# Optimization experiments

Hardware: AMD Instinct MI355X
Metric: run time of the kernel (lower is better)

Reference implementation:

```python
import jax, jax.numpy as jnp
import numpy as np

SIGMA = 25.0
N, E, F, D = 10000, 160000, 256, 3


def setup_inputs() -> dict:
    key = jax.random.key(0)
    ks = jax.random.split(key, 24)
    s = 0.02
    inp = {
        "x": jax.random.normal(ks[0], (N, D), jnp.float32),
        "edge_index": jax.random.randint(ks[1], (2, E), 0, N, jnp.int64),
        "t": jax.random.uniform(ks[2], (N, 1), jnp.float32, 1e-3, 1.0),
        "emb_pcs": jax.random.normal(ks[3], (N, F), jnp.float32),
        # x_encoder
        "enc_W": jax.random.normal(ks[4], (D, F), jnp.float32) * s,
        "enc_b": jnp.zeros((F,), jnp.float32),
        # GaussianFourierProjection (scale=30, fixed) + Linear
        "fourier_W": jax.random.normal(ks[5], (F // 2,), jnp.float32) * 30.0,
        "te_W": jax.random.normal(ks[6], (F, F), jnp.float32) * s,
        "te_b": jnp.zeros((F,), jnp.float32),
        # mlp1 / mlp2: Linear(6F,F) -> ReLU -> Linear(F,F)
        "m1_W1": jax.random.normal(ks[7], (6 * F, F), jnp.float32) * s,
        "m1_b1": jnp.zeros((F,), jnp.float32),
        "m1_W2": jax.random.normal(ks[8], (F, F), jnp.float32) * s,
        "m1_b2": jnp.zeros((F,), jnp.float32),
        "m2_W1": jax.random.normal(ks[9], (6 * F, F), jnp.float32) * s,
        "m2_b1": jnp.zeros((F,), jnp.float32),
        "m2_W2": jax.random.normal(ks[10], (F, F), jnp.float32) * s,
        "m2_b2": jnp.zeros((F,), jnp.float32),
        # mlp3: Linear(6F,F) -> ReLU -> Linear(F,D)
        "m3_W1": jax.random.normal(ks[11], (6 * F, F), jnp.float32) * s,
        "m3_b1": jnp.zeros((F,), jnp.float32),
        "m3_W2": jax.random.normal(ks[12], (F, D), jnp.float32) * s,
        "m3_b2": jnp.zeros((D,), jnp.float32),
    }
    return inp


def _edge_conv(h, src, dst, W1, b1, W2, b2, n):
    # PyG EdgeConv: out_i = max_{j->i} MLP([x_i, x_j - x_i])
    hi = h[dst]                                             # [E, 3F]
    e = jnp.concatenate([hi, h[src] - hi], axis=-1)         # [E, 6F]
    e = jax.nn.relu(e @ W1 + b1) @ W2 + b2                  # [E, out]
    out = jax.ops.segment_max(e, dst, num_segments=n)
    return jnp.where(jnp.isfinite(out), out, 0.0)           # empty segments -> 0


def reference(x, edge_index, t, emb_pcs,
              enc_W, enc_b, fourier_W, te_W, te_b,
              m1_W1, m1_b1, m1_W2, m1_b2,
              m2_W1, m2_b1, m2_W2, m2_b2,
              m3_W1, m3_b1, m3_W2, m3_b2):
    src, dst = edge_index[0], edge_index[1]
    n = x.shape[0]
    # time embedding: Fourier projection -> Linear -> swish
    tv = t[:, 0]
    proj = tv[:, None] * fourier_W[None, :] * (2.0 * np.pi)  # [N, F/2]
    temb = jnp.concatenate([jnp.sin(proj), jnp.cos(proj)], axis=-1) @ te_W + te_b
    temb = temb * jax.nn.sigmoid(temb)                       # [N, F]
    h = x @ enc_W + enc_b                                    # [N, F]
    h = jnp.concatenate([h, temb, emb_pcs], axis=-1)         # [N, 3F]
    h = jax.nn.relu(_edge_conv(h, src, dst, m1_W1, m1_b1, m1_W2, m1_b2, n))
    h = jnp.concatenate([h, temb, emb_pcs], axis=-1)
    h = jax.nn.relu(_edge_conv(h, src, dst, m2_W1, m2_b1, m2_W2, m2_b2, n))
    h = jnp.concatenate([h, temb, emb_pcs], axis=-1)
    h = _edge_conv(h, src, dst, m3_W1, m3_b1, m3_W2, m3_b2, n)  # [N, D]
    # marginal_prob_std(t) = sqrt((sigma^(2t) - 1) / (2 ln sigma))
    std = jnp.sqrt((jnp.power(SIGMA, 2.0 * t) - 1.0) / (2.0 * jnp.log(SIGMA)))
    return h / (std + 1e-7)
```

## Files before the change

kernel.cpp:

```cpp
#include <hip/hip_runtime.h>
#include <hip/hip_bf16.h>
#include <math.h>

#define HC 768
#define DPB 8

typedef __attribute__((ext_vector_type(8))) short bf16x8;
typedef __attribute__((ext_vector_type(4))) float f32x4;

__device__ __forceinline__ float bf2f(unsigned short h) {
    return __uint_as_float(((unsigned)h) << 16);
}
__device__ __forceinline__ unsigned short f2bf(float f) {
    unsigned u = __float_as_uint(f);
    return (unsigned short)((u + 0x7fffu + ((u >> 16) & 1u)) >> 16);
}
__device__ __forceinline__ unsigned pack_bf2(float a, float b) {
    __hip_bfloat162 h = __float22bfloat162_rn(make_float2(a, b));
    return *reinterpret_cast<unsigned*>(&h);
}

__device__ __forceinline__ unsigned enc_f(float f) {
    unsigned u = __float_as_uint(f);
    return (u & 0x80000000u) ? ~u : (u | 0x80000000u);
}
__device__ __forceinline__ float dec_f(unsigned e) {
    unsigned u = (e & 0x80000000u) ? (e & 0x7FFFFFFFu) : ~e;
    return __uint_as_float(u);
}
#define ENC_NEG_INF 0x007FFFFFu

__global__ void pre_and_prep_kernel(const float* __restrict__ x,
                                    const float* __restrict__ t,
                                    const float* __restrict__ emb,
                                    const float* __restrict__ enc_W,
                                    const float* __restrict__ enc_b,
                                    const float* __restrict__ fw,
                                    const float* __restrict__ te_W,
                                    const float* __restrict__ te_b,
                                    unsigned short* __restrict__ hcat,
                                    float* __restrict__ invstd,
                                    const float* __restrict__ W1a,
                                    const float* __restrict__ W1b,
                                    const float* __restrict__ W1c,
                                    const float* __restrict__ W2a,
                                    const float* __restrict__ W2b,
                                    const float* __restrict__ W2c,
                                    unsigned short* __restrict__ WcatT,
                                    unsigned short* __restrict__ W2T,
                                    unsigned short* __restrict__ W2T3,
                                    int N, int nPre) {
    __shared__ float smem[64 * 65];
    const int tid = threadIdx.x;

    if ((int)blockIdx.x < nPre) {
        float (*ti)[256] = (float(*)[256])smem;
        float* tv = smem + 8 * 256;
        const int n0 = blockIdx.x * 8;

        if (tid < 8) {
            int n = n0 + tid;
            float tt = (n < N) ? t[n] : 1.0f;
            tv[tid] = tt;
            const float ln_s = 3.2188758248682006f;
            float p = expf(2.0f * tt * ln_s);
            float sd = sqrtf((p - 1.0f) / (2.0f * ln_s));
            if (n < N) invstd[n] = 1.0f / (sd + 1e-7f);
        }
        __syncthreads();

        const float TWO_PI = 6.283185307179586f;
        for (int p = tid; p < 8 * 128; p += 256) {
            int n = p >> 7, j = p & 127;
            float pr = tv[n] * fw[j] * TWO_PI;
            ti[n][j]       = sinf(pr);
            ti[n][j + 128] = cosf(pr);
        }
        __syncthreads();

        const int j = tid;
        float acc[8];
#pragma unroll
        for (int n = 0; n < 8; ++n) acc[n] = 0.f;
        for (int k = 0; k < 256; ++k) {
            float w = te_W[k * 256 + j];
#pragma unroll
            for (int n = 0; n < 8; ++n) acc[n] += ti[n][k] * w;
        }
        float bj  = te_b[j];
        float ew0 = enc_W[0 * 256 + j], ew1 = enc_W[1 * 256 + j], ew2 = enc_W[2 * 256 + j];
        float ebj = enc_b[j];
        for (int n = 0; n < 8; ++n) {
            int node = n0 + n;
            if (node >= N) break;
            float v = acc[n] + bj;
            float temb = v / (1.0f + expf(-v));
            float h0 = x[node * 3 + 0] * ew0 + x[node * 3 + 1] * ew1 +
                       x[node * 3 + 2] * ew2 + ebj;
            hcat[(size_t)node * HC + j]       = f2bf(h0);
            hcat[(size_t)node * HC + 256 + j] = f2bf(temb);
            hcat[(size_t)node * HC + 512 + j] = f2bf(emb[node * 256 + j]);
        }
    } else {
        float (*buf)[65] = (float(*)[65])smem;
        const int bid = blockIdx.x - nPre;
        const int tx = tid & 63, ty = tid >> 6;

        if (bid < 288) {
            const int l = bid / 96, r = bid - l * 96;
            const float* W1 = (l == 0) ? W1a : (l == 1) ? W1b : W1c;
            unsigned short* WT = WcatT + (size_t)l * 512 * 768;
            const int k0 = (r % 12) * 64, n0 = (r / 12) * 64;
#pragma unroll
            for (int i = 0; i < 16; ++i) {
                int kl = ty + i * 4;
                int k = k0 + kl, n = n0 + tx;
                float v = (n < 256) ? (W1[(size_t)k * 256 + n] - W1[(size_t)(k + 768) * 256 + n])
                                    : W1[(size_t)(k + 768) * 256 + (n - 256)];
                buf[kl][tx] = v;
            }
            __syncthreads();
#pragma unroll
            for (int i = 0; i < 16; ++i) {
                int nl = ty + i * 4;
                WT[(size_t)(n0 + nl) * 768 + k0 + tx] = f2bf(buf[tx][nl]);
            }
        } else if (bid < 320) {
            const int m = bid - 288, l = m >> 4, r = m & 15;
            const float* W2 = (l == 0) ? W2a : W2b;
            unsigned short* WT = W2T + (size_t)l * 256 * 256;
            const int k0 = (r & 3) * 64, n0 = (r >> 2) * 64;
#pragma unroll
            for (int i = 0; i < 16; ++i) {
                int kl = ty + i * 4;
                buf[kl][tx] = W2[(size_t)(k0 + kl) * 256 + n0 + tx];
            }
            __syncthreads();
#pragma unroll
            for (int i = 0; i < 16; ++i) {
                int nl = ty + i * 4;
                WT[(size_t)(n0 + nl) * 256 + k0 + tx] = f2bf(buf[tx][nl]);
            }
        } else {
            int idx = (bid - 320) * 256 + tid;
            int n = idx >> 8, k = idx & 255;
            W2T3[idx] = (n < 3) ? f2bf(W2c[(size_t)k * 3 + n]) : (unsigned short)0;
        }
    }
}

__global__ __launch_bounds__(256)
void node_gemm_mfma_kernel(const unsigned short* __restrict__ A,
                           const unsigned short* __restrict__ BT,
                           const float* __restrict__ b1,
                           unsigned short* __restrict__ C,
                           int M) {
    const int row0 = blockIdx.x * 64, col0 = blockIdx.y * 128;
    const int tid = threadIdx.x;
    const int wv = tid >> 6, lane = tid & 63;
    const int q = lane >> 4, nl = lane & 15;

    int row = row0 + wv * 16 + nl;
    int rowc = (row < M) ? row : (M - 1);
    const unsigned short* pa = A + (size_t)rowc * HC + q * 8;

    f32x4 acc[8];
#pragma unroll
    for (int t = 0; t < 8; ++t) acc[t] = (f32x4){0.f, 0.f, 0.f, 0.f};

    for (int ks = 0; ks < 24; ++ks) {
        const int k0 = ks * 32;
        const bf16x8 av = *(const bf16x8*)(pa + k0);
#pragma unroll
        for (int t = 0; t < 8; ++t) {
            const bf16x8 bv = *(const bf16x8*)(BT + (size_t)(col0 + t * 16 + nl) * 768 + k0 + q * 8);
            acc[t] = __builtin_amdgcn_mfma_f32_16x16x32_bf16(av, bv, acc[t], 0, 0, 0);
        }
    }

    const int r0 = row0 + wv * 16 + q * 4;
#pragma unroll
    for (int t = 0; t < 8; ++t) {
        int col = col0 + t * 16 + nl;
        float bb = (col < 256) ? b1[col] : 0.f;
#pragma unroll
        for (int i = 0; i < 4; ++i) {
            int r = r0 + i;
            if (r < M) C[(size_t)r * 512 + col] = f2bf(acc[t][i] + bb);
        }
    }
}

__global__ void init_kernel(unsigned* __restrict__ cnt, unsigned* __restrict__ seg3, int N) {
    int idx = blockIdx.x * 256 + threadIdx.x;
    if (idx < 2 * N) cnt[idx] = 0u;
    else if (idx < 5 * N) seg3[idx - 2 * N] = ENC_NEG_INF;
}
__global__ void hist_kernel(const int* __restrict__ dst, unsigned* __restrict__ cnt, int E) {
    int e = blockIdx.x * 256 + threadIdx.x;
    if (e < E) atomicAdd(&cnt[dst[e]], 1u);
}
__global__ void scan_kernel(const unsigned* __restrict__ cnt,
                            int* __restrict__ row_start, int N) {
    __shared__ unsigned buf[1024];
    __shared__ unsigned carry;
    const int tid = threadIdx.x;
    if (tid == 0) carry = 0u;
    __syncthreads();
    for (int base = 0; base < N; base += 1024) {
        int i = base + tid;
        unsigned v = (i < N) ? cnt[i] : 0u;
        buf[tid] = v;
        __syncthreads();
#pragma unroll
        for (int off = 1; off < 1024; off <<= 1) {
            unsigned add = (tid >= off) ? buf[tid - off] : 0u;
            __syncthreads();
            buf[tid] += add;
            __syncthreads();
        }
        if (i < N) row_start[i] = (int)(carry + buf[tid] - v);
        __syncthreads();
        if (tid == 0) carry += buf[1023];
        __syncthreads();
    }
    if (tid == 0) row_start[N] = (int)carry;
}
__global__ void scatter_kernel(const int* __restrict__ src, const int* __restrict__ dst,
                               const int* __restrict__ row_start,
                               unsigned* __restrict__ wcnt,
                               int* __restrict__ es, int* __restrict__ ed, int E) {
    int e = blockIdx.x * 256 + threadIdx.x;
    if (e >= E) return;
    int d = dst[e];
    int pos = row_start[d] + (int)atomicAdd(&wcnt[d], 1u);
    es[pos] = src[e];
    ed[pos] = d;
}

__global__ __launch_bounds__(256, 3)
void edge_seg_gemm_kernel(const unsigned short* __restrict__ RQb,
                          const int* __restrict__ es,
                          const int* __restrict__ ed,
                          const int* __restrict__ row_start,
                          const unsigned short* __restrict__ W2T,
                          const float* __restrict__ b2,
                          unsigned short* __restrict__ hcat,
                          int N, int E) {
    __shared__ unsigned short af2[32 * 64 * 8];
    __shared__ unsigned short rdst[DPB][264];
    __shared__ unsigned lseg[DPB * 256];
    __shared__ int ss[64], sdl[64];
    const int d0 = blockIdx.x * DPB;
    const int tid = threadIdx.x;
    const int wv = tid >> 6, lane = tid & 63;
    const int q = lane >> 4, nl = lane & 15;

    for (int i = tid; i < DPB * 256; i += 256) lseg[i] = ENC_NEG_INF;

    {
        int rrow = tid >> 5;
        int kc = (tid & 31) * 8;
        int d = d0 + rrow;
        int dc = (d < N) ? d : (N - 1);
        *(bf16x8*)&rdst[rrow][kc] = *(const bf16x8*)(RQb + (size_t)dc * 512 + kc);
    }

    const int eBeg = row_start[d0];
    const int eEnd = row_start[min(d0 + DPB, N)];

    for (int c0 = eBeg; c0 < eEnd; c0 += 64) {
        __syncthreads();
        if (tid < 64) {
            int e = c0 + tid;
            ss[tid]  = (e < eEnd) ? es[e] : 0;
            sdl[tid] = (e < eEnd) ? (ed[e] - d0) : -1;
        }
        __syncthreads();

        {
            const int el = tid >> 2;
            const int kc = (tid & 3) * 64;
            int dl = sdl[el];
            int dla = (dl >= 0) ? dl : 0;
            int srow = ss[el];
            const unsigned short* ps = RQb + (size_t)srow * 512 + 256;
#pragma unroll
            for (int j = 0; j < 8; ++j) {
                const int k = kc + j * 8;
                bf16x8 dv = *(const bf16x8*)&rdst[dla][k];
                bf16x8 sv = *(const bf16x8*)(ps + k);
                float f[8];
#pragma unroll
                for (int u = 0; u < 8; ++u)
                    f[u] = fmaxf(bf2f((unsigned short)dv[u]) + bf2f((unsigned short)sv[u]), 0.f);
                uint4 o;
                o.x = pack_bf2(f[0], f[1]);
                o.y = pack_bf2(f[2], f[3]);
                o.z = pack_bf2(f[4], f[5]);
                o.w = pack_bf2(f[6], f[7]);
                *(uint4*)&af2[((k >> 3) * 64 + el) * 8] = o;
            }
        }
        __syncthreads();

#pragma unroll
        for (int sub = 0; sub < 4; ++sub) {
            f32x4 acc[4];
#pragma unroll
            for (int t = 0; t < 4; ++t) acc[t] = (f32x4){0.f, 0.f, 0.f, 0.f};
#pragma unroll
            for (int ks = 0; ks < 8; ++ks) {
                const bf16x8 av = *(const bf16x8*)&af2[((ks * 4 + q) * 64 + sub * 16 + nl) * 8];
#pragma unroll
                for (int t = 0; t < 4; ++t) {
                    const bf16x8 bv = *(const bf16x8*)(W2T +
                        (size_t)(wv * 64 + t * 16 + nl) * 256 + ks * 32 + q * 8);
                    acc[t] = __builtin_amdgcn_mfma_f32_16x16x32_bf16(av, bv, acc[t], 0, 0, 0);
                }
            }
            const int m0 = sub * 16 + q * 4;
            int dls[4];
#pragma unroll
            for (int i = 0; i < 4; ++i) dls[i] = sdl[m0 + i];
#pragma unroll
            for (int t = 0; t < 4; ++t) {
                const int col = wv * 64 + t * 16 + nl;
                float cur = -INFINITY;
                int cd = dls[0];
#pragma unroll
                for (int i = 0; i < 4; ++i) {
                    int dl = dls[i];
                    if (dl != cd) {
                        if (cd >= 0) atomicMax(&lseg[cd * 256 + col], enc_f(cur));
                        cur = -INFINITY; cd = dl;
                    }
                    cur = fmaxf(cur, acc[t][i]);
                }
                if (cd >= 0) atomicMax(&lseg[cd * 256 + col], enc_f(cur));
            }
        }
    }
    __syncthreads();

    for (int i = tid; i < DPB * 256; i += 256) {
        int dl = i >> 8, col = i & 255;
        int d = d0 + dl;
        if (d >= N) continue;
        float f = dec_f(lseg[i]);
        float v = isfinite(f) ? fmaxf(f + b2[col], 0.f) : 0.f;
        hcat[(size_t)d * HC + col] = f2bf(v);
    }
}

__global__ __launch_bounds__(256)
void edge3_mfma_kernel(const unsigned short* __restrict__ RQb,
                       const int* __restrict__ es,
                       const int* __restrict__ ed,
                       const unsigned short* __restrict__ W2T3,
                       const float* __restrict__ b2,
                       unsigned* __restrict__ seg3,
                       int E) {
    const int wave = blockIdx.x * 4 + (threadIdx.x >> 6);
    const int lane = threadIdx.x & 63;
    const int q = lane >> 4, nl = lane & 15;
    const int e0 = wave * 16;
    if (e0 >= E) return;

    bf16x8 bv[8];
#pragma unroll
    for (int ks = 0; ks < 8; ++ks)
        bv[ks] = *(const bf16x8*)(W2T3 + (size_t)nl * 256 + ks * 32 + q * 8);

    int eA = e0 + nl;
    int eAc = (eA < E) ? eA : (E - 1);
    const int dA = ed[eAc], sA = es[eAc];
    const unsigned short* pd = RQb + (size_t)dA * 512 + q * 8;
    const unsigned short* ps = RQb + (size_t)sA * 512 + 256 + q * 8;

    f32x4 acc = (f32x4){0.f, 0.f, 0.f, 0.f};
#pragma unroll
    for (int ks = 0; ks < 8; ++ks) {
        bf16x8 dv = *(const bf16x8*)(pd + ks * 32);
        bf16x8 sv = *(const bf16x8*)(ps + ks * 32);
        float f[8];
#pragma unroll
        for (int u = 0; u < 8; ++u)
            f[u] = fmaxf(bf2f((unsigned short)dv[u]) + bf2f((unsigned short)sv[u]), 0.f);
        uint4 o;
        o.x = pack_bf2(f[0], f[1]);
        o.y = pack_bf2(f[2], f[3]);
        o.z = pack_bf2(f[4], f[5]);
        o.w = pack_bf2(f[6], f[7]);
        bf16x8 av = *(bf16x8*)&o;
        acc = __builtin_amdgcn_mfma_f32_16x16x32_bf16(av, bv[ks], acc, 0, 0, 0);
    }

    if (nl < 3) {
        float bb = b2[nl];
        float cur = -INFINITY;
        int cd = -2;
#pragma unroll
        for (int i = 0; i < 4; ++i) {
            int e = e0 + q * 4 + i;
            int d = (e < E) ? ed[e] : -1;
            if (d != cd) {
                if (cd >= 0) atomicMax(&seg3[(size_t)cd * 3 + nl], enc_f(cur + bb));
                cur = -INFINITY; cd = d;
            }
            if (d >= 0) cur = fmaxf(cur, acc[i]);
        }
        if (cd >= 0) atomicMax(&seg3[(size_t)cd * 3 + nl], enc_f(cur + bb));
    }
}

__global__ void finalize3_kernel(const unsigned* __restrict__ seg3,
                                 const float* __restrict__ invstd,
                                 float* __restrict__ out, int N) {
    int idx = blockIdx.x * 256 + threadIdx.x;
    if (idx >= N * 3) return;
    int n = idx / 3;
    float f = dec_f(seg3[idx]);
    if (!isfinite(f)) f = 0.f;
    out[idx] = f * invstd[n];
}

extern "C" void kernel_launch(void* const* d_in, const int* in_sizes, int n_in,
                              void* d_out, int out_size, void* d_ws, size_t ws_size,
                              hipStream_t stream) {
    const float* x     = (const float*)d_in[0];
    const int*   ei    = (const int*)d_in[1];
    const float* t     = (const float*)d_in[2];
    const float* emb   = (const float*)d_in[3];
    const float* enc_W = (const float*)d_in[4];
    const float* enc_b = (const float*)d_in[5];
    const float* fw    = (const float*)d_in[6];
    const float* te_W  = (const float*)d_in[7];
    const float* te_b  = (const float*)d_in[8];
    const float* W1[3] = {(const float*)d_in[9],  (const float*)d_in[13], (const float*)d_in[17]};
    const float* b1[3] = {(const float*)d_in[10], (const float*)d_in[14], (const float*)d_in[18]};
    const float* W2[3] = {(const float*)d_in[11], (const float*)d_in[15], (const float*)d_in[19]};
    const float* b2[3] = {(const float*)d_in[12], (const float*)d_in[16], (const float*)d_in[20]};

    const int N = in_sizes[2];
    const int E = in_sizes[1] / 2;
    const int* src = ei;
    const int* dst = ei + E;

    char* ws = (char*)d_ws;
    unsigned short* hcat  = (unsigned short*)ws; ws += (size_t)N * HC * 2;
    unsigned short* RQb   = (unsigned short*)ws; ws += (size_t)N * 512 * 2;
    unsigned short* WcatT = (unsigned short*)ws; ws += (size_t)3 * 512 * 768 * 2;
    unsigned short* W2T   = (unsigned short*)ws; ws += (size_t)2 * 256 * 256 * 2;
    unsigned short* W2T3  = (unsigned short*)ws; ws += (size_t)16 * 256 * 2;
    unsigned* seg3        = (unsigned*)ws;       ws += (size_t)N * 3 * 4;
    float*    invstd      = (float*)ws;          ws += (size_t)N * 4;
    int*      es          = (int*)ws;            ws += (size_t)E * 4;
    int*      ed          = (int*)ws;            ws += (size_t)E * 4;
    unsigned* cnt         = (unsigned*)ws;       ws += (size_t)N * 4;
    unsigned* wcnt        = (unsigned*)ws;       ws += (size_t)N * 4;
    int*      row_start   = (int*)ws;            ws += (size_t)(N + 1) * 4;

    init_kernel<<<(5 * N + 255) / 256, 256, 0, stream>>>(cnt, seg3, N);
    hist_kernel<<<(E + 255) / 256, 256, 0, stream>>>(dst, cnt, E);
    scan_kernel<<<1, 1024, 0, stream>>>(cnt, row_start, N);
    scatter_kernel<<<(E + 255) / 256, 256, 0, stream>>>(src, dst, row_start, wcnt, es, ed, E);

    const int nPre = (N + 7) / 8;
    pre_and_prep_kernel<<<nPre + 336, 256, 0, stream>>>(
        x, t, emb, enc_W, enc_b, fw, te_W, te_b, hcat, invstd,
        W1[0], W1[1], W1[2], W2[0], W2[1], W2[2], WcatT, W2T, W2T3, N, nPre);

    for (int l = 0; l < 3; ++l) {
        dim3 gn((N + 63) / 64, 4);
        node_gemm_mfma_kernel<<<gn, 256, 0, stream>>>(
            hcat, WcatT + (size_t)l * 512 * 768, b1[l], RQb, N);
        if (l < 2) {
            edge_seg_gemm_kernel<<<(N + DPB - 1) / DPB, 256, 0, stream>>>(
                RQb, es, ed, row_start, W2T + (size_t)l * 256 * 256, b2[l], hcat, N, E);
        } else {
            int chunks = (E + 15) / 16;
            edge3_mfma_kernel<<<(chunks + 3) / 4, 256, 0, stream>>>(
                RQb, es, ed, W2T3, b2[l], seg3, E);
            finalize3_kernel<<<(N * 3 + 255) / 256, 256, 0, stream>>>(seg3, invstd, (float*)d_out, N);
        }
    }
}
```

Before: 590.7 us.

## Retile node GEMM waves to 32x64 and pad edge-tile LDS to row-major

The node GEMM now gives each wave a 32x64 output tile instead of 16x128. Each B fragment load feeds two MFMAs, so global B traffic per block is halved at the cost of one extra A load. The edge kernel's LDS staging buffer switches from a k-chunk-major layout to a row-major layout padded to 264 columns. The padding is meant to avoid bank conflicts when A fragments are read by row, and the rdst padding is dropped. Register pressure in the node GEMM stays about the same.

```diff
diff --git a/kernel.cpp b/kernel.cpp
--- a/kernel.cpp
+++ b/kernel.cpp
@@ -159,34 +159,44 @@
     const int tid = threadIdx.x;
     const int wv = tid >> 6, lane = tid & 63;
     const int q = lane >> 4, nl = lane & 15;
-
-    int row = row0 + wv * 16 + nl;
-    int rowc = (row < M) ? row : (M - 1);
-    const unsigned short* pa = A + (size_t)rowc * HC + q * 8;
-
-    f32x4 acc[8];
-#pragma unroll
-    for (int t = 0; t < 8; ++t) acc[t] = (f32x4){0.f, 0.f, 0.f, 0.f};
+    const int rbase = row0 + (wv >> 1) * 32;
+    const int cbase = col0 + (wv & 1) * 64;
+
+    int r0c = min(rbase + nl, M - 1);
+    int r1c = min(rbase + 16 + nl, M - 1);
+    const unsigned short* pa0 = A + (size_t)r0c * HC + q * 8;
+    const unsigned short* pa1 = A + (size_t)r1c * HC + q * 8;
+
+    f32x4 acc[2][4];
+#pragma unroll
+    for (int s = 0; s < 2; ++s)
+#pragma unroll
+        for (int t = 0; t < 4; ++t) acc[s][t] = (f32x4){0.f, 0.f, 0.f, 0.f};
 
     for (int ks = 0; ks < 24; ++ks) {
         const int k0 = ks * 32;
-        const bf16x8 av = *(const bf16x8*)(pa + k0);
-#pragma unroll
-        for (int t = 0; t < 8; ++t) {
-            const bf16x8 bv = *(const bf16x8*)(BT + (size_t)(col0 + t * 16 + nl) * 768 + k0 + q * 8);
-            acc[t] = __builtin_amdgcn_mfma_f32_16x16x32_bf16(av, bv, acc[t], 0, 0, 0);
-        }
-    }
-
-    const int r0 = row0 + wv * 16 + q * 4;
-#pragma unroll
-    for (int t = 0; t < 8; ++t) {
-        int col = col0 + t * 16 + nl;
-        float bb = (col < 256) ? b1[col] : 0.f;
-#pragma unroll
-        for (int i = 0; i < 4; ++i) {
-            int r = r0 + i;
-            if (r < M) C[(size_t)r * 512 + col] = f2bf(acc[t][i] + bb);
+        const bf16x8 av0 = *(const bf16x8*)(pa0 + k0);
+        const bf16x8 av1 = *(const bf16x8*)(pa1 + k0);
+#pragma unroll
+        for (int t = 0; t < 4; ++t) {
+            const bf16x8 bv = *(const bf16x8*)(BT + (size_t)(cbase + t * 16 + nl) * 768 + k0 + q * 8);
+            acc[0][t] = __builtin_amdgcn_mfma_f32_16x16x32_bf16(av0, bv, acc[0][t], 0, 0, 0);
+            acc[1][t] = __builtin_amdgcn_mfma_f32_16x16x32_bf16(av1, bv, acc[1][t], 0, 0, 0);
+        }
+    }
+
+#pragma unroll
+    for (int s = 0; s < 2; ++s) {
+        const int rr = rbase + s * 16 + q * 4;
+#pragma unroll
+        for (int t = 0; t < 4; ++t) {
+            int col = cbase + t * 16 + nl;
+            float bb = (col < 256) ? b1[col] : 0.f;
+#pragma unroll
+            for (int i = 0; i < 4; ++i) {
+                int r = rr + i;
+                if (r < M) C[(size_t)r * 512 + col] = f2bf(acc[s][t][i] + bb);
+            }
         }
     }
 }
@@ -247,8 +257,8 @@
                           const float* __restrict__ b2,
                           unsigned short* __restrict__ hcat,
                           int N, int E) {
-    __shared__ unsigned short af2[32 * 64 * 8];
-    __shared__ unsigned short rdst[DPB][264];
+    __shared__ unsigned short af[64][264];
+    __shared__ unsigned short rdst[DPB][256];
     __shared__ unsigned lseg[DPB * 256];
     __shared__ int ss[64], sdl[64];
     const int d0 = blockIdx.x * DPB;
@@ -284,12 +294,11 @@
             int dl = sdl[el];
             int dla = (dl >= 0) ? dl : 0;
             int srow = ss[el];
-            const unsigned short* ps = RQb + (size_t)srow * 512 + 256;
+            const unsigned short* ps = RQb + (size_t)srow * 512 + 256 + kc;
 #pragma unroll
             for (int j = 0; j < 8; ++j) {
-                const int k = kc + j * 8;
-                bf16x8 dv = *(const bf16x8*)&rdst[dla][k];
-                bf16x8 sv = *(const bf16x8*)(ps + k);
+                bf16x8 dv = *(const bf16x8*)&rdst[dla][kc + j * 8];
+                bf16x8 sv = *(const bf16x8*)(ps + j * 8);
                 float f[8];
 #pragma unroll
                 for (int u = 0; u < 8; ++u)
@@ -299,7 +308,7 @@
                 o.y = pack_bf2(f[2], f[3]);
                 o.z = pack_bf2(f[4], f[5]);
                 o.w = pack_bf2(f[6], f[7]);
-                *(uint4*)&af2[((k >> 3) * 64 + el) * 8] = o;
+                *(uint4*)&af[el][kc + j * 8] = o;
             }
         }
         __syncthreads();
@@ -311,7 +320,7 @@
             for (int t = 0; t < 4; ++t) acc[t] = (f32x4){0.f, 0.f, 0.f, 0.f};
 #pragma unroll
             for (int ks = 0; ks < 8; ++ks) {
-                const bf16x8 av = *(const bf16x8*)&af2[((ks * 4 + q) * 64 + sub * 16 + nl) * 8];
+                const bf16x8 av = *(const bf16x8*)&af[sub * 16 + nl][ks * 32 + q * 8];
 #pragma unroll
                 for (int t = 0; t < 4; ++t) {
                     const bf16x8 bv = *(const bf16x8*)(W2T +
```

Result: faster. 503.0 us (-14.8%).
